# Kernel tuning notes

Hardware: AMD Instinct MI355X
Metric: run time of the kernel (lower is better)

Reference implementation:

```python
import jax, jax.numpy as jnp
import numpy as np

N_ENTITIES = 200000
N_EDGES = 1200000
N_RELATIONS = 32
LATDIM = 64
N_HOPS = 2
RES_LAMBDA = 0.5  # args.res_lambda
LEAKY_SLOPE = 0.2
EPS = 1e-12


def setup_inputs() -> dict:
    key = jax.random.key(0)
    k1, k2, k3, k4, k5 = jax.random.split(key, 5)
    entity_emb = jax.random.normal(k1, (N_ENTITIES, LATDIM), dtype=jnp.float32)
    relation_emb = jax.random.normal(k2, (N_RELATIONS, LATDIM), dtype=jnp.float32)
    W = jax.random.normal(k3, (2 * LATDIM, LATDIM), dtype=jnp.float32) * (1.0 / np.sqrt(2 * LATDIM))
    edge_index = jax.random.randint(k4, (2, N_EDGES), 0, N_ENTITIES, dtype=jnp.int64)
    edge_type = jax.random.randint(k5, (N_EDGES,), 0, N_RELATIONS, dtype=jnp.int64)
    return {"entity_emb": entity_emb, "relation_emb": relation_emb, "W": W,
            "edge_index": edge_index, "edge_type": edge_type}


def _l2_normalize(x):
    # F.normalize(x) : row-wise L2 normalize with eps clamp
    n = jnp.sqrt(jnp.sum(x * x, axis=-1, keepdims=True))
    return x / jnp.maximum(n, EPS)


def _agg(entity_emb, relation_emb, W, head, tail, edge_type):
    n = entity_emb.shape[0]
    # gather head/tail embeddings -> [E, 2*D]
    a_input = jnp.concatenate([entity_emb[head], entity_emb[tail]], axis=-1)
    # attention logit per edge: ((a_input @ W) * r_e).sum(-1)
    e = jnp.sum((a_input @ W) * relation_emb[edge_type], axis=-1)
    e = jax.nn.leaky_relu(e, LEAKY_SLOPE)
    # scatter_softmax over edges grouped by head node
    m = jax.ops.segment_max(e, head, num_segments=n)
    ex = jnp.exp(e - m[head])
    denom = jax.ops.segment_sum(ex, head, num_segments=n)
    alpha = ex / denom[head]
    # scatter_sum of alpha-weighted tail embeddings
    agg_emb = jax.ops.segment_sum(entity_emb[tail] * alpha[:, None], head, num_segments=n)
    return agg_emb + entity_emb


def reference(entity_emb, relation_emb, W, edge_index, edge_type):
    head, tail = edge_index[0], edge_index[1]
    entity_res_emb = entity_emb
    ent = entity_emb
    for _ in range(N_HOPS):
        ent = _agg(ent, relation_emb, W, head, tail, edge_type)
        ent = _l2_normalize(ent)  # mess_dropout disabled (deterministic reference)
        entity_res_emb = RES_LAMBDA * entity_res_emb + ent
    return entity_res_emb
```

## Files before the change

kernel.cpp:

```cpp
#include <hip/hip_runtime.h>
#include <hip/hip_bf16.h>


#define N_ENT  200000
#define N_EDGE 1200000
#define N_REL  32
#define DIM    64
#define LEAKY  0.2f
#define CAP    32
#define NBIN   (CAP + 1)
#define SUBH   500
#define NSUB   (N_ENT / SUBH)
#define SQCAP  3500
#define I4PB   2048
#define NRB    ((N_EDGE / 4 + I4PB - 1) / I4PB)

template <int CTRL>
__device__ __forceinline__ float dpp_add(float x) {
  int t = __builtin_amdgcn_update_dpp(0, __float_as_int(x), CTRL, 0xF, 0xF, true);
  return x + __int_as_float(t);
}
__device__ __forceinline__ float red16(float x) {
  x = dpp_add<0xB1>(x);
  x = dpp_add<0x4E>(x);
  x = dpp_add<0x124>(x);
  x = dpp_add<0x128>(x);
  return x;
}

__device__ __forceinline__ float4 unpack4(uint2 u) {
  float4 t;
  t.x = __uint_as_float(u.x << 16);
  t.y = __uint_as_float(u.x & 0xFFFF0000u);
  t.z = __uint_as_float(u.y << 16);
  t.w = __uint_as_float(u.y & 0xFFFF0000u);
  return t;
}
__device__ __forceinline__ unsigned pk(float a, float b) {
  unsigned ua = __float_as_uint(a);
  ua += 0x7FFFu + ((ua >> 16) & 1u);
  unsigned ub = __float_as_uint(b);
  ub += 0x7FFFu + ((ub >> 16) & 1u);
  return (ua >> 16) | (ub & 0xFFFF0000u);
}

__global__ __launch_bounds__(256) void preproute(
    const float* __restrict__ W, const float* __restrict__ R,
    float* __restrict__ Q,
    const float4* __restrict__ ent04, uint2* __restrict__ ent0b,
    const int4* __restrict__ head4, const int4* __restrict__ tail4,
    const int4* __restrict__ type4,
    int* __restrict__ sqcnt, uint2* __restrict__ sqdata) {
  __shared__ int lcnt[NSUB];
  __shared__ int lbase[NSUB];
  __shared__ int lrank[NSUB];
  if (blockIdx.x < NRB) {
    for (int i = threadIdx.x; i < NSUB; i += blockDim.x) {
      lcnt[i] = 0;
      lrank[i] = 0;
    }
    __syncthreads();
    int base = blockIdx.x * I4PB;
    int lim = min(N_EDGE / 4, base + I4PB);
    for (int k = base + threadIdx.x; k < lim; k += blockDim.x) {
      int4 h = head4[k];
      atomicAdd(&lcnt[h.x / SUBH], 1);
      atomicAdd(&lcnt[h.y / SUBH], 1);
      atomicAdd(&lcnt[h.z / SUBH], 1);
      atomicAdd(&lcnt[h.w / SUBH], 1);
    }
    __syncthreads();
    for (int i = threadIdx.x; i < NSUB; i += blockDim.x)
      if (lcnt[i] > 0) lbase[i] = atomicAdd(&sqcnt[i], lcnt[i]);
    __syncthreads();
    for (int k = base + threadIdx.x; k < lim; k += blockDim.x) {
      int4 h = head4[k];
      int4 t = tail4[k];
      int4 r = type4[k];
      int s, p;
      s = h.x / SUBH; p = lbase[s] + atomicAdd(&lrank[s], 1);
      if (p < SQCAP) sqdata[(size_t)s * SQCAP + p] =
          make_uint2((unsigned)t.x | ((unsigned)r.x << 18), (unsigned)h.x);
      s = h.y / SUBH; p = lbase[s] + atomicAdd(&lrank[s], 1);
      if (p < SQCAP) sqdata[(size_t)s * SQCAP + p] =
          make_uint2((unsigned)t.y | ((unsigned)r.y << 18), (unsigned)h.y);
      s = h.z / SUBH; p = lbase[s] + atomicAdd(&lrank[s], 1);
      if (p < SQCAP) sqdata[(size_t)s * SQCAP + p] =
          make_uint2((unsigned)t.z | ((unsigned)r.z << 18), (unsigned)h.z);
      s = h.w / SUBH; p = lbase[s] + atomicAdd(&lrank[s], 1);
      if (p < SQCAP) sqdata[(size_t)s * SQCAP + p] =
          make_uint2((unsigned)t.w | ((unsigned)r.w << 18), (unsigned)h.w);
    }
  }
  int tid = blockIdx.x * blockDim.x + threadIdx.x;
  int stride = gridDim.x * blockDim.x;
  for (int i = tid; i < N_REL * 2 * DIM; i += stride) {
    int r = i >> 7;
    int k = i & 127;
    float acc = 0.f;
#pragma unroll 8
    for (int j = 0; j < DIM; ++j)
      acc += W[k * DIM + j] * R[r * DIM + j];
    Q[i] = acc;
  }
  for (int i = tid; i < N_ENT * DIM / 4; i += stride) {
    float4 v = ent04[i];
    ent0b[i] = make_uint2(pk(v.x, v.y), pk(v.z, v.w));
  }
}

__global__ __launch_bounds__(256) void fill3s(
    const int* __restrict__ sqcnt,
    const uint2* __restrict__ sqdata,
    unsigned* __restrict__ bucket,
    unsigned* __restrict__ order) {
  __shared__ unsigned lbucket[SUBH * CAP];
  __shared__ int lcur[SUBH];
  __shared__ int lbin[NBIN];
  __shared__ int lbs[NBIN];
  __shared__ int lrk[NBIN];
  int g = blockIdx.x;
  int hbase = g * SUBH;
  for (int i = threadIdx.x; i < SUBH; i += blockDim.x) lcur[i] = 0;
  if (threadIdx.x < NBIN) { lbin[threadIdx.x] = 0; lrk[threadIdx.x] = 0; }
  __syncthreads();
  int n = min(sqcnt[g], SQCAP);
  const uint2* q = sqdata + (size_t)g * SQCAP;
  for (int k = threadIdx.x; k < n; k += blockDim.x) {
    uint2 rec = q[k];
    int lh = (int)rec.y - hbase;
    int p = atomicAdd(&lcur[lh], 1);
    if (p < CAP) lbucket[lh * CAP + p] = rec.x;
  }
  __syncthreads();
  const uint4* lb4 = (const uint4*)lbucket;
  uint4* gb4 = (uint4*)(bucket + (size_t)hbase * CAP);
  for (int i = threadIdx.x; i < SUBH * CAP / 4; i += blockDim.x) gb4[i] = lb4[i];
  for (int i = threadIdx.x; i < SUBH; i += blockDim.x)
    atomicAdd(&lbin[min(lcur[i], CAP)], 1);
  __syncthreads();
  if (threadIdx.x == 0) {
    int s = 0;
    for (int b = 0; b < NBIN; ++b) { lbs[b] = s; s += lbin[b]; }
  }
  __syncthreads();
  for (int i = threadIdx.x; i < SUBH; i += blockDim.x) {
    int d = min(lcur[i], CAP);
    int slot = lbs[d] + atomicAdd(&lrk[d], 1);
    order[(size_t)slot * NSUB + g] = (unsigned)(hbase + i) | ((unsigned)d << 18);
  }
}

template <int HOP>
__global__ __launch_bounds__(256, 8) void hop_kernel(
    const ushort* __restrict__ entb,
    const ushort* __restrict__ e0b,
    const float4* __restrict__ Qg,
    const unsigned* __restrict__ order,
    const unsigned* __restrict__ bucket,
    uint2* __restrict__ outb,
    float* __restrict__ outf) {
  __shared__ float4 sQ[N_REL * 32];
  for (int i = threadIdx.x; i < N_REL * 32; i += blockDim.x) sQ[i] = Qg[i];
  __syncthreads();
  const int lane = threadIdx.x & 63;
  const int sub = lane & 15;
  const int grp = lane >> 4;
  const int wave = (blockIdx.x * blockDim.x + threadIdx.x) >> 6;
  const int nWaves = (gridDim.x * blockDim.x) >> 6;
  const uint2* gtab = (const uint2*)entb;
  for (int n4 = wave * 4; n4 < N_ENT; n4 += nWaves * 4) {
    unsigned oe = order[n4 + grp];
    int n = (int)(oe & 0x3FFFFu);
    int len = (int)(oe >> 18);
    float4 eh = unpack4(gtab[(size_t)n * 16 + sub]);
    int b = n * CAP;
    float l = 0.f;
    float4 acc = make_float4(0.f, 0.f, 0.f, 0.f);
    unsigned p0 = 0u, p1 = 0u, p2 = 0u;
    uint2 t0 = make_uint2(0u, 0u), t1 = t0, t2 = t0;
    if (0 < len) { p0 = bucket[b];     t0 = gtab[(size_t)(p0 & 0x3FFFFu) * 16 + sub]; }
    if (1 < len) { p1 = bucket[b + 1]; t1 = gtab[(size_t)(p1 & 0x3FFFFu) * 16 + sub]; }
    if (2 < len) { p2 = bucket[b + 2]; t2 = gtab[(size_t)(p2 & 0x3FFFFu) * 16 + sub]; }
    for (int i = 0; __any(i < len); ++i) {
      unsigned p3 = 0u;
      uint2 t3 = make_uint2(0u, 0u);
      if (i + 3 < len) { p3 = bucket[b + i + 3];
                         t3 = gtab[(size_t)(p3 & 0x3FFFFu) * 16 + sub]; }
      if (i < len) {
        int r = (int)(p0 >> 18);
        float4 qh = sQ[r * 32 + sub];
        float4 qt = sQ[r * 32 + 16 + sub];
        float4 et = unpack4(t0);
        float d = eh.x * qh.x + eh.y * qh.y + eh.z * qh.z + eh.w * qh.w
                + et.x * qt.x + et.y * qt.y + et.z * qt.z + et.w * qt.w;
        d = red16(d);
        float v = d > 0.f ? d : LEAKY * d;
        float ex = __expf(v);
        l += ex;
        acc.x = fmaf(ex, et.x, acc.x);
        acc.y = fmaf(ex, et.y, acc.y);
        acc.z = fmaf(ex, et.z, acc.z);
        acc.w = fmaf(ex, et.w, acc.w);
      }
      p0 = p1; t0 = t1; p1 = p2; t1 = t2; p2 = p3; t2 = t3;
    }
    float inv = (l > 0.f) ? 1.f / l : 0.f;
    float4 v;
    v.x = fmaf(acc.x, inv, eh.x);
    v.y = fmaf(acc.y, inv, eh.y);
    v.z = fmaf(acc.z, inv, eh.z);
    v.w = fmaf(acc.w, inv, eh.w);
    float s = v.x * v.x + v.y * v.y + v.z * v.z + v.w * v.w;
    s = red16(s);
    float rn = 1.f / fmaxf(sqrtf(s), 1e-12f);
    if (HOP == 1) {
      outb[(size_t)n * 16 + sub] = make_uint2(pk(v.x * rn, v.y * rn),
                                              pk(v.z * rn, v.w * rn));
    } else {
      float4 e0 = unpack4(((const uint2*)e0b)[(size_t)n * 16 + sub]);
      float4 o;
      o.x = fmaf(0.25f, e0.x, fmaf(0.5f, eh.x, v.x * rn));
      o.y = fmaf(0.25f, e0.y, fmaf(0.5f, eh.y, v.y * rn));
      o.z = fmaf(0.25f, e0.z, fmaf(0.5f, eh.z, v.z * rn));
      o.w = fmaf(0.25f, e0.w, fmaf(0.5f, eh.w, v.w * rn));
      ((float4*)(outf + (size_t)n * DIM))[sub] = o;
    }
  }
}

extern "C" void kernel_launch(void* const* d_in, const int* in_sizes, int n_in,
                              void* d_out, int out_size, void* d_ws, size_t ws_size,
                              hipStream_t stream) {
  const float* ent0 = (const float*)d_in[0];
  const float* rel  = (const float*)d_in[1];
  const float* W    = (const float*)d_in[2];
  const int* edge_index = (const int*)d_in[3];
  const int* etype      = (const int*)d_in[4];
  const int* head = edge_index;
  const int* tail = edge_index + N_EDGE;
  float* out = (float*)d_out;

  char* ws = (char*)d_ws;
  float*    Q      = (float*)ws;
  unsigned* bucket = (unsigned*)(ws + 16384);
  ushort*   ent0b  = (ushort*)(ws + 16384 + 25600000);
  ushort*   h1b    = (ushort*)(ws + 16384 + 51200000);
  unsigned* order  = (unsigned*)(ws + 16384 + 76800000);
  int*      sqcnt  = (int*)(ws + 16384 + 77600000);
  uint2*    sqdata = (uint2*)h1b;

  hipMemsetAsync(sqcnt, 0, NSUB * sizeof(int), stream);
  preproute<<<2048, 256, 0, stream>>>(
      W, rel, Q, (const float4*)ent0, (uint2*)ent0b,
      (const int4*)head, (const int4*)tail, (const int4*)etype,
      sqcnt, sqdata);
  fill3s<<<NSUB, 256, 0, stream>>>(sqcnt, sqdata, bucket, order);
  hop_kernel<1><<<2048, 256, 0, stream>>>(ent0b, nullptr, (const float4*)Q,
                                          order, bucket, (uint2*)h1b, nullptr);
  hop_kernel<2><<<2048, 256, 0, stream>>>(h1b, ent0b, (const float4*)Q,
                                          order, bucket, nullptr, out);
}
```

Baseline: 238.1 us.

## Compact per-node edge buckets into CSR-style array and shorten prefetch depth

Replaces the fixed-capacity padded bucket array (CAP slots per node) with a compacted edge list, where each sub-block reserves space through a global atomic counter and stores per-node offsets in an expanded order record. This shrinks the fill kernel's write traffic and the workspace footprint. The hop kernel reads the edge offset from the order entry and its software prefetch depth drops from three edges to two, which cuts register pressure. The cost is a serial prefix scan by one thread per block, scalar uncoalesced per-node copies, and an extra 4 bytes per order entry.

```diff
diff --git a/kernel.cpp b/kernel.cpp
--- a/kernel.cpp
+++ b/kernel.cpp
@@ -112,13 +112,16 @@
 __global__ __launch_bounds__(256) void fill3s(
     const int* __restrict__ sqcnt,
     const uint2* __restrict__ sqdata,
-    unsigned* __restrict__ bucket,
-    unsigned* __restrict__ order) {
+    unsigned* __restrict__ edges,
+    uint2* __restrict__ order2,
+    int* __restrict__ ecnt) {
   __shared__ unsigned lbucket[SUBH * CAP];
   __shared__ int lcur[SUBH];
+  __shared__ int lpref[SUBH];
   __shared__ int lbin[NBIN];
   __shared__ int lbs[NBIN];
   __shared__ int lrk[NBIN];
+  __shared__ int gbase;
   int g = blockIdx.x;
   int hbase = g * SUBH;
   for (int i = threadIdx.x; i < SUBH; i += blockDim.x) lcur[i] = 0;
@@ -133,9 +136,17 @@
     if (p < CAP) lbucket[lh * CAP + p] = rec.x;
   }
   __syncthreads();
-  const uint4* lb4 = (const uint4*)lbucket;
-  uint4* gb4 = (uint4*)(bucket + (size_t)hbase * CAP);
-  for (int i = threadIdx.x; i < SUBH * CAP / 4; i += blockDim.x) gb4[i] = lb4[i];
+  if (threadIdx.x == 0) {
+    int s = 0;
+    for (int i = 0; i < SUBH; ++i) { lpref[i] = s; s += min(lcur[i], CAP); }
+    gbase = atomicAdd(ecnt, s);
+  }
+  __syncthreads();
+  for (int i = threadIdx.x; i < SUBH; i += blockDim.x) {
+    int d = min(lcur[i], CAP);
+    int dst = gbase + lpref[i];
+    for (int k = 0; k < d; ++k) edges[dst + k] = lbucket[i * CAP + k];
+  }
   for (int i = threadIdx.x; i < SUBH; i += blockDim.x)
     atomicAdd(&lbin[min(lcur[i], CAP)], 1);
   __syncthreads();
@@ -147,7 +158,9 @@
   for (int i = threadIdx.x; i < SUBH; i += blockDim.x) {
     int d = min(lcur[i], CAP);
     int slot = lbs[d] + atomicAdd(&lrk[d], 1);
-    order[(size_t)slot * NSUB + g] = (unsigned)(hbase + i) | ((unsigned)d << 18);
+    order2[(size_t)slot * NSUB + g] =
+        make_uint2((unsigned)(hbase + i) | ((unsigned)d << 18),
+                   (unsigned)(gbase + lpref[i]));
   }
 }
 
@@ -156,8 +169,8 @@
     const ushort* __restrict__ entb,
     const ushort* __restrict__ e0b,
     const float4* __restrict__ Qg,
-    const unsigned* __restrict__ order,
-    const unsigned* __restrict__ bucket,
+    const uint2* __restrict__ order2,
+    const unsigned* __restrict__ edges,
     uint2* __restrict__ outb,
     float* __restrict__ outf) {
   __shared__ float4 sQ[N_REL * 32];
@@ -170,23 +183,22 @@
   const int nWaves = (gridDim.x * blockDim.x) >> 6;
   const uint2* gtab = (const uint2*)entb;
   for (int n4 = wave * 4; n4 < N_ENT; n4 += nWaves * 4) {
-    unsigned oe = order[n4 + grp];
-    int n = (int)(oe & 0x3FFFFu);
-    int len = (int)(oe >> 18);
+    uint2 oe = order2[n4 + grp];
+    int n = (int)(oe.x & 0x3FFFFu);
+    int len = (int)(oe.x >> 18);
+    int b = (int)oe.y;
     float4 eh = unpack4(gtab[(size_t)n * 16 + sub]);
-    int b = n * CAP;
     float l = 0.f;
     float4 acc = make_float4(0.f, 0.f, 0.f, 0.f);
-    unsigned p0 = 0u, p1 = 0u, p2 = 0u;
-    uint2 t0 = make_uint2(0u, 0u), t1 = t0, t2 = t0;
-    if (0 < len) { p0 = bucket[b];     t0 = gtab[(size_t)(p0 & 0x3FFFFu) * 16 + sub]; }
-    if (1 < len) { p1 = bucket[b + 1]; t1 = gtab[(size_t)(p1 & 0x3FFFFu) * 16 + sub]; }
-    if (2 < len) { p2 = bucket[b + 2]; t2 = gtab[(size_t)(p2 & 0x3FFFFu) * 16 + sub]; }
+    unsigned p0 = 0u, p1 = 0u;
+    uint2 t0 = make_uint2(0u, 0u), t1 = t0;
+    if (0 < len) { p0 = edges[b];     t0 = gtab[(size_t)(p0 & 0x3FFFFu) * 16 + sub]; }
+    if (1 < len) { p1 = edges[b + 1]; t1 = gtab[(size_t)(p1 & 0x3FFFFu) * 16 + sub]; }
     for (int i = 0; __any(i < len); ++i) {
-      unsigned p3 = 0u;
-      uint2 t3 = make_uint2(0u, 0u);
-      if (i + 3 < len) { p3 = bucket[b + i + 3];
-                         t3 = gtab[(size_t)(p3 & 0x3FFFFu) * 16 + sub]; }
+      unsigned p2 = 0u;
+      uint2 t2 = make_uint2(0u, 0u);
+      if (i + 2 < len) { p2 = edges[b + i + 2];
+                         t2 = gtab[(size_t)(p2 & 0x3FFFFu) * 16 + sub]; }
       if (i < len) {
         int r = (int)(p0 >> 18);
         float4 qh = sQ[r * 32 + sub];
@@ -203,7 +215,7 @@
         acc.z = fmaf(ex, et.z, acc.z);
         acc.w = fmaf(ex, et.w, acc.w);
       }
-      p0 = p1; t0 = t1; p1 = p2; t1 = t2; p2 = p3; t2 = t3;
+      p0 = p1; t0 = t1; p1 = p2; t1 = t2;
     }
     float inv = (l > 0.f) ? 1.f / l : 0.f;
     float4 v;
@@ -243,21 +255,22 @@
 
   char* ws = (char*)d_ws;
   float*    Q      = (float*)ws;
-  unsigned* bucket = (unsigned*)(ws + 16384);
-  ushort*   ent0b  = (ushort*)(ws + 16384 + 25600000);
-  ushort*   h1b    = (ushort*)(ws + 16384 + 51200000);
-  unsigned* order  = (unsigned*)(ws + 16384 + 76800000);
-  int*      sqcnt  = (int*)(ws + 16384 + 77600000);
+  unsigned* edges  = (unsigned*)(ws + 16384);
+  ushort*   ent0b  = (ushort*)(ws + 16384 + 4800000);
+  ushort*   h1b    = (ushort*)(ws + 16384 + 30400000);
+  uint2*    order2 = (uint2*)(ws + 16384 + 56000000);
+  int*      sqcnt  = (int*)(ws + 16384 + 57600000);
+  int*      ecnt   = (int*)(ws + 16384 + 57601600);
   uint2*    sqdata = (uint2*)h1b;
 
-  hipMemsetAsync(sqcnt, 0, NSUB * sizeof(int), stream);
+  hipMemsetAsync(sqcnt, 0, NSUB * sizeof(int) + 64, stream);
   preproute<<<2048, 256, 0, stream>>>(
       W, rel, Q, (const float4*)ent0, (uint2*)ent0b,
       (const int4*)head, (const int4*)tail, (const int4*)etype,
       sqcnt, sqdata);
-  fill3s<<<NSUB, 256, 0, stream>>>(sqcnt, sqdata, bucket, order);
+  fill3s<<<NSUB, 256, 0, stream>>>(sqcnt, sqdata, edges, order2, ecnt);
   hop_kernel<1><<<2048, 256, 0, stream>>>(ent0b, nullptr, (const float4*)Q,
-                                          order, bucket, (uint2*)h1b, nullptr);
+                                          order2, edges, (uint2*)h1b, nullptr);
   hop_kernel<2><<<2048, 256, 0, stream>>>(h1b, ent0b, (const float4*)Q,
-                                          order, bucket, nullptr, out);
-}
+                                          order2, edges, nullptr, out);
+}
```

Result: slower. 245.8 us (+3.2%).

## Replace global-atomic edge routing with per-block fixed-capacity chunks, shorten prefetch depth

Applied to the files above, without the earlier changes.

The edge-routing preprocess no longer does a counting pass plus global atomics to reserve space in per-subrange queues. Each routing block now writes its edges straight into a private fixed-capacity chunk per subrange and stores a 2D count table. fill3s then walks those chunks wave by wave. This removes one head-index read pass, the global atomics and the memset, but any block/subrange with more than 48 edges silently drops the extras. The hop kernel's software prefetch depth is also reduced from three to two edges ahead to lower register pressure.

```diff
diff --git a/kernel.cpp b/kernel.cpp
--- a/kernel.cpp
+++ b/kernel.cpp
@@ -11,9 +11,9 @@
 #define NBIN   (CAP + 1)
 #define SUBH   500
 #define NSUB   (N_ENT / SUBH)
-#define SQCAP  3500
 #define I4PB   2048
 #define NRB    ((N_EDGE / 4 + I4PB - 1) / I4PB)
+#define CAPC   48
 
 template <int CTRL>
 __device__ __forceinline__ float dpp_add(float x) {
@@ -50,47 +50,34 @@
     const float4* __restrict__ ent04, uint2* __restrict__ ent0b,
     const int4* __restrict__ head4, const int4* __restrict__ tail4,
     const int4* __restrict__ type4,
-    int* __restrict__ sqcnt, uint2* __restrict__ sqdata) {
+    int* __restrict__ qcnt2d, uint2* __restrict__ sqdata) {
   __shared__ int lcnt[NSUB];
-  __shared__ int lbase[NSUB];
-  __shared__ int lrank[NSUB];
   if (blockIdx.x < NRB) {
-    for (int i = threadIdx.x; i < NSUB; i += blockDim.x) {
-      lcnt[i] = 0;
-      lrank[i] = 0;
-    }
+    for (int i = threadIdx.x; i < NSUB; i += blockDim.x) lcnt[i] = 0;
     __syncthreads();
     int base = blockIdx.x * I4PB;
     int lim = min(N_EDGE / 4, base + I4PB);
     for (int k = base + threadIdx.x; k < lim; k += blockDim.x) {
       int4 h = head4[k];
-      atomicAdd(&lcnt[h.x / SUBH], 1);
-      atomicAdd(&lcnt[h.y / SUBH], 1);
-      atomicAdd(&lcnt[h.z / SUBH], 1);
-      atomicAdd(&lcnt[h.w / SUBH], 1);
-    }
-    __syncthreads();
-    for (int i = threadIdx.x; i < NSUB; i += blockDim.x)
-      if (lcnt[i] > 0) lbase[i] = atomicAdd(&sqcnt[i], lcnt[i]);
-    __syncthreads();
-    for (int k = base + threadIdx.x; k < lim; k += blockDim.x) {
-      int4 h = head4[k];
       int4 t = tail4[k];
       int4 r = type4[k];
       int s, p;
-      s = h.x / SUBH; p = lbase[s] + atomicAdd(&lrank[s], 1);
-      if (p < SQCAP) sqdata[(size_t)s * SQCAP + p] =
+      s = h.x / SUBH; p = atomicAdd(&lcnt[s], 1);
+      if (p < CAPC) sqdata[((size_t)s * NRB + blockIdx.x) * CAPC + p] =
           make_uint2((unsigned)t.x | ((unsigned)r.x << 18), (unsigned)h.x);
-      s = h.y / SUBH; p = lbase[s] + atomicAdd(&lrank[s], 1);
-      if (p < SQCAP) sqdata[(size_t)s * SQCAP + p] =
+      s = h.y / SUBH; p = atomicAdd(&lcnt[s], 1);
+      if (p < CAPC) sqdata[((size_t)s * NRB + blockIdx.x) * CAPC + p] =
           make_uint2((unsigned)t.y | ((unsigned)r.y << 18), (unsigned)h.y);
-      s = h.z / SUBH; p = lbase[s] + atomicAdd(&lrank[s], 1);
-      if (p < SQCAP) sqdata[(size_t)s * SQCAP + p] =
+      s = h.z / SUBH; p = atomicAdd(&lcnt[s], 1);
+      if (p < CAPC) sqdata[((size_t)s * NRB + blockIdx.x) * CAPC + p] =
           make_uint2((unsigned)t.z | ((unsigned)r.z << 18), (unsigned)h.z);
-      s = h.w / SUBH; p = lbase[s] + atomicAdd(&lrank[s], 1);
-      if (p < SQCAP) sqdata[(size_t)s * SQCAP + p] =
+      s = h.w / SUBH; p = atomicAdd(&lcnt[s], 1);
+      if (p < CAPC) sqdata[((size_t)s * NRB + blockIdx.x) * CAPC + p] =
           make_uint2((unsigned)t.w | ((unsigned)r.w << 18), (unsigned)h.w);
     }
+    __syncthreads();
+    for (int i = threadIdx.x; i < NSUB; i += blockDim.x)
+      qcnt2d[i * NRB + blockIdx.x] = min(lcnt[i], CAPC);
   }
   int tid = blockIdx.x * blockDim.x + threadIdx.x;
   int stride = gridDim.x * blockDim.x;
@@ -110,27 +97,34 @@
 }
 
 __global__ __launch_bounds__(256) void fill3s(
-    const int* __restrict__ sqcnt,
+    const int* __restrict__ qcnt2d,
     const uint2* __restrict__ sqdata,
     unsigned* __restrict__ bucket,
     unsigned* __restrict__ order) {
   __shared__ unsigned lbucket[SUBH * CAP];
   __shared__ int lcur[SUBH];
+  __shared__ int ccnt[NRB];
   __shared__ int lbin[NBIN];
   __shared__ int lbs[NBIN];
   __shared__ int lrk[NBIN];
   int g = blockIdx.x;
   int hbase = g * SUBH;
   for (int i = threadIdx.x; i < SUBH; i += blockDim.x) lcur[i] = 0;
+  for (int i = threadIdx.x; i < NRB; i += blockDim.x) ccnt[i] = qcnt2d[g * NRB + i];
   if (threadIdx.x < NBIN) { lbin[threadIdx.x] = 0; lrk[threadIdx.x] = 0; }
   __syncthreads();
-  int n = min(sqcnt[g], SQCAP);
-  const uint2* q = sqdata + (size_t)g * SQCAP;
-  for (int k = threadIdx.x; k < n; k += blockDim.x) {
-    uint2 rec = q[k];
-    int lh = (int)rec.y - hbase;
-    int p = atomicAdd(&lcur[lh], 1);
-    if (p < CAP) lbucket[lh * CAP + p] = rec.x;
+  const uint2* qg = sqdata + (size_t)g * NRB * CAPC;
+  int wid = threadIdx.x >> 6;
+  int ln = threadIdx.x & 63;
+  for (int b = wid; b < NRB; b += 4) {
+    int c = ccnt[b];
+    const uint2* qc = qg + b * CAPC;
+    for (int j = ln; j < c; j += 64) {
+      uint2 rec = qc[j];
+      int lh = (int)rec.y - hbase;
+      int p = atomicAdd(&lcur[lh], 1);
+      if (p < CAP) lbucket[lh * CAP + p] = rec.x;
+    }
   }
   __syncthreads();
   const uint4* lb4 = (const uint4*)lbucket;
@@ -177,16 +171,15 @@
     int b = n * CAP;
     float l = 0.f;
     float4 acc = make_float4(0.f, 0.f, 0.f, 0.f);
-    unsigned p0 = 0u, p1 = 0u, p2 = 0u;
-    uint2 t0 = make_uint2(0u, 0u), t1 = t0, t2 = t0;
+    unsigned p0 = 0u, p1 = 0u;
+    uint2 t0 = make_uint2(0u, 0u), t1 = t0;
     if (0 < len) { p0 = bucket[b];     t0 = gtab[(size_t)(p0 & 0x3FFFFu) * 16 + sub]; }
     if (1 < len) { p1 = bucket[b + 1]; t1 = gtab[(size_t)(p1 & 0x3FFFFu) * 16 + sub]; }
-    if (2 < len) { p2 = bucket[b + 2]; t2 = gtab[(size_t)(p2 & 0x3FFFFu) * 16 + sub]; }
     for (int i = 0; __any(i < len); ++i) {
-      unsigned p3 = 0u;
-      uint2 t3 = make_uint2(0u, 0u);
-      if (i + 3 < len) { p3 = bucket[b + i + 3];
-                         t3 = gtab[(size_t)(p3 & 0x3FFFFu) * 16 + sub]; }
+      unsigned p2 = 0u;
+      uint2 t2 = make_uint2(0u, 0u);
+      if (i + 2 < len) { p2 = bucket[b + i + 2];
+                         t2 = gtab[(size_t)(p2 & 0x3FFFFu) * 16 + sub]; }
       if (i < len) {
         int r = (int)(p0 >> 18);
         float4 qh = sQ[r * 32 + sub];
@@ -203,7 +196,7 @@
         acc.z = fmaf(ex, et.z, acc.z);
         acc.w = fmaf(ex, et.w, acc.w);
       }
-      p0 = p1; t0 = t1; p1 = p2; t1 = t2; p2 = p3; t2 = t3;
+      p0 = p1; t0 = t1; p1 = p2; t1 = t2;
     }
     float inv = (l > 0.f) ? 1.f / l : 0.f;
     float4 v;
@@ -247,15 +240,14 @@
   ushort*   ent0b  = (ushort*)(ws + 16384 + 25600000);
   ushort*   h1b    = (ushort*)(ws + 16384 + 51200000);
   unsigned* order  = (unsigned*)(ws + 16384 + 76800000);
-  int*      sqcnt  = (int*)(ws + 16384 + 77600000);
+  int*      qcnt2d = (int*)(ws + 16384 + 77600000);
   uint2*    sqdata = (uint2*)h1b;
 
-  hipMemsetAsync(sqcnt, 0, NSUB * sizeof(int), stream);
   preproute<<<2048, 256, 0, stream>>>(
       W, rel, Q, (const float4*)ent0, (uint2*)ent0b,
       (const int4*)head, (const int4*)tail, (const int4*)etype,
-      sqcnt, sqdata);
-  fill3s<<<NSUB, 256, 0, stream>>>(sqcnt, sqdata, bucket, order);
+      qcnt2d, sqdata);
+  fill3s<<<NSUB, 256, 0, stream>>>(qcnt2d, sqdata, bucket, order);
   hop_kernel<1><<<2048, 256, 0, stream>>>(ent0b, nullptr, (const float4*)Q,
                                           order, bucket, (uint2*)h1b, nullptr);
   hop_kernel<2><<<2048, 256, 0, stream>>>(h1b, ent0b, (const float4*)Q,
```

Result: slower. 253.8 us (+6.6%).
